# Optimization experiments

Measured on AMD Instinct MI355X. Metric: run time of the kernel, lower is better.

The kernel has to match this reference:

```python
import jax, jax.numpy as jnp
import numpy as np

N_NODES = 100000
N_EDGES = 500000
D = 128          # node / edge latent size
HIDDEN = 128     # MLP hidden width


def setup_inputs() -> dict:
    key = jax.random.key(0)
    k = jax.random.split(key, 10)
    node_attr = jax.random.normal(k[0], (N_NODES, D), dtype=jnp.float32)
    edge_attr = jax.random.normal(k[1], (N_EDGES, D), dtype=jnp.float32)
    senders_idx = jax.random.randint(k[2], (N_EDGES,), 0, N_NODES, dtype=jnp.int64 if jax.config.jax_enable_x64 else jnp.int32).astype(jnp.int32)
    receivers_idx = jax.random.randint(k[3], (N_EDGES,), 0, N_NODES).astype(jnp.int32)
    in_dim = 3 * D  # sender + receiver + edge feats
    s1 = 1.0 / np.sqrt(in_dim)
    s2 = 1.0 / np.sqrt(HIDDEN)
    W1 = jax.random.uniform(k[4], (in_dim, HIDDEN), minval=-s1, maxval=s1, dtype=jnp.float32)
    b1 = jnp.zeros((HIDDEN,), jnp.float32)
    W2 = jax.random.uniform(k[5], (HIDDEN, D), minval=-s2, maxval=s2, dtype=jnp.float32)
    b2 = jnp.zeros((D,), jnp.float32)
    ln_gamma = jnp.ones((D,), jnp.float32)
    ln_beta = jnp.zeros((D,), jnp.float32)
    return {
        "node_attr": node_attr, "edge_attr": edge_attr,
        "senders_idx": senders_idx, "receivers_idx": receivers_idx,
        "W1": W1, "b1": b1, "W2": W2, "b2": b2,
        "ln_gamma": ln_gamma, "ln_beta": ln_beta,
    }


def _layer_norm(x, gamma, beta, eps=1e-5):
    mu = jnp.mean(x, axis=-1, keepdims=True)
    var = jnp.var(x, axis=-1, keepdims=True)
    return (x - mu) * jax.lax.rsqrt(var + eps) * gamma + beta


def reference(node_attr, edge_attr, senders_idx, receivers_idx,
              W1, b1, W2, b2, ln_gamma, ln_beta):
    # Gather sender/receiver node features  [E, D] each
    senders_attr = node_attr[senders_idx]
    receivers_attr = node_attr[receivers_idx]
    # Concat -> [E, 3D]
    collected = jnp.concatenate([senders_attr, receivers_attr, edge_attr], axis=1)
    # MLP with ReLU + output LayerNorm (MeshGraphNets custom_func)
    h = jax.nn.relu(collected @ W1 + b1)
    out = h @ W2 + b2
    new_edge_attr = _layer_norm(out, ln_gamma, ln_beta)
    return new_edge_attr
```

## Files before the change

kernel.cpp:

```cpp
#include <hip/hip_runtime.h>

#define D 128
#define NEDGES 500000
#define NNODES 100000

typedef short short8 __attribute__((ext_vector_type(8)));
typedef float f32x4 __attribute__((ext_vector_type(4)));
typedef unsigned short us4 __attribute__((ext_vector_type(4)));
typedef unsigned short us8 __attribute__((ext_vector_type(8)));

static __device__ __forceinline__ unsigned short f2bf(float f) {
  unsigned u = __builtin_bit_cast(unsigned, f);
  u += 0x7fff + ((u >> 16) & 1);
  return (unsigned short)(u >> 16);
}

static __device__ __forceinline__ unsigned short f2h(float f) {
  return __builtin_bit_cast(unsigned short, (_Float16)f);
}

static __device__ __forceinline__ float h2f(unsigned short u) {
  return (float)__builtin_bit_cast(_Float16, u);
}

static __device__ __forceinline__ short8 cvt8v(f32x4 a, f32x4 b) {
  short8 r;
  r[0] = (short)f2bf(a[0]); r[1] = (short)f2bf(a[1]);
  r[2] = (short)f2bf(a[2]); r[3] = (short)f2bf(a[3]);
  r[4] = (short)f2bf(b[0]); r[5] = (short)f2bf(b[1]);
  r[6] = (short)f2bf(b[2]); r[7] = (short)f2bf(b[3]);
  return r;
}

__global__ void prep_weights2(const float* __restrict__ W1,
                              const float* __restrict__ W2,
                              unsigned short* __restrict__ WnS,
                              unsigned short* __restrict__ WnR,
                              unsigned short* __restrict__ WnE,
                              unsigned short* __restrict__ Wt2) {
  int tid = blockIdx.x * 256 + threadIdx.x;
  int seg = tid >> 14;
  int t = tid & 16383;
  int unit = t >> 7;
  int k = t & 127;
  if (seg == 0)      WnS[t] = f2bf(W1[k * 128 + unit]);
  else if (seg == 1) WnR[t] = f2bf(W1[(128 + k) * 128 + unit]);
  else if (seg == 2) WnE[t] = f2bf(W1[(256 + k) * 128 + unit]);
  else {
    int kk = k >> 5, rem = k & 31, q = rem >> 3, s = rem & 7;
    int keff = ((s < 4) ? (2 * kk) : (2 * kk + 1)) * 16 + q * 4 + (s & 3);
    Wt2[t] = f2bf(W2[keff * 128 + unit]);
  }
}

__global__ __launch_bounds__(512) void node_proj(
    const float* __restrict__ node,
    const unsigned short* __restrict__ WnS,
    const unsigned short* __restrict__ WnR,
    unsigned short* __restrict__ Ps,
    unsigned short* __restrict__ Pr) {
  __shared__ __align__(16) unsigned short wlds[2][16384];
  {
    const us8* s0 = (const us8*)WnS;
    const us8* s1 = (const us8*)WnR;
#pragma unroll
    for (int c = 0; c < 4; ++c) {
      int g = threadIdx.x + c * 512;
      int row = g >> 4, slot = g & 15;
      int dst = row * 128 + ((slot ^ (row & 7)) << 3);
      *(us8*)&wlds[0][dst] = s0[g];
      *(us8*)&wlds[1][dst] = s1[g];
    }
  }
  __syncthreads();

  const int lane = threadIdx.x & 63;
  const int wave = threadIdx.x >> 6;
  const int col = lane & 15;
  const int quad = lane >> 4;
  const int c7 = col & 7;
  const int nBase = blockIdx.x * 128 + wave * 16;
  if (nBase >= NNODES) return;

  const float* src = node + (size_t)(nBase + col) * D + quad * 8;
  f32x4 c[4][2];
#pragma unroll
  for (int kk = 0; kk < 4; ++kk) {
    c[kk][0] = __builtin_nontemporal_load((const f32x4*)(src + kk * 32));
    c[kk][1] = __builtin_nontemporal_load((const f32x4*)(src + kk * 32 + 4));
  }
  f32x4 accS[8], accR[8];
  const f32x4 zero = {0.f, 0.f, 0.f, 0.f};
#pragma unroll
  for (int m = 0; m < 8; ++m) { accS[m] = zero; accR[m] = zero; }

#pragma unroll
  for (int kk = 0; kk < 4; ++kk) {
    short8 bf = cvt8v(c[kk][0], c[kk][1]);
#pragma unroll
    for (int m = 0; m < 8; ++m) {
      const int off = (m * 16 + col) * 128 + (((kk * 4 + quad) ^ c7) << 3);
      short8 as = *(const short8*)&wlds[0][off];
      accS[m] = __builtin_amdgcn_mfma_f32_16x16x32_bf16(as, bf, accS[m], 0, 0, 0);
      short8 ar = *(const short8*)&wlds[1][off];
      accR[m] = __builtin_amdgcn_mfma_f32_16x16x32_bf16(ar, bf, accR[m], 0, 0, 0);
    }
  }

  unsigned short* ps = Ps + (size_t)(nBase + col) * D + quad * 32;
  unsigned short* pr = Pr + (size_t)(nBase + col) * D + quad * 32;
#pragma unroll
  for (int m = 0; m < 8; m += 2) {
    us8 w1v, w2v;
#pragma unroll
    for (int r = 0; r < 4; ++r) {
      w1v[r] = f2h(accS[m][r]);     w1v[4 + r] = f2h(accS[m + 1][r]);
      w2v[r] = f2h(accR[m][r]);     w2v[4 + r] = f2h(accR[m + 1][r]);
    }
    *(us8*)(ps + m * 4) = w1v;
    *(us8*)(pr + m * 4) = w2v;
  }
}

__global__ __launch_bounds__(512) void edge_mlp(
    const float* __restrict__ edge,
    const int* __restrict__ send, const int* __restrict__ recv,
    const unsigned short* __restrict__ WnE,
    const unsigned short* __restrict__ Wt2,
    const unsigned short* __restrict__ Ps,
    const unsigned short* __restrict__ Pr,
    const float* __restrict__ b1, const float* __restrict__ b2,
    const float* __restrict__ gamma, const float* __restrict__ beta,
    float* __restrict__ out) {
  __shared__ __align__(16) unsigned short wlds[2][16384];
  {
    const us8* s0 = (const us8*)WnE;
    const us8* s1 = (const us8*)Wt2;
#pragma unroll
    for (int c = 0; c < 4; ++c) {
      int g = threadIdx.x + c * 512;
      int row = g >> 4, slot = g & 15;
      int dst = row * 128 + ((slot ^ (row & 7)) << 3);
      *(us8*)&wlds[0][dst] = s0[g];
      *(us8*)&wlds[1][dst] = s1[g];
    }
  }
  __syncthreads();

  const int lane = threadIdx.x & 63;
  const int wave = threadIdx.x >> 6;
  const int col = lane & 15;
  const int quad = lane >> 4;
  const int q4 = quad * 4;
  const int c7 = col & 7;
  const int eBase = blockIdx.x * 128 + wave * 16;
  if (eBase >= NEDGES) return;

  const int e = eBase + col;
  const int si = send[e];
  const int ri = recv[e];

  const float* ge = edge + (size_t)e * D + quad * 8;
  f32x4 c[4][2];
#pragma unroll
  for (int kk = 0; kk < 4; ++kk) {
    c[kk][0] = __builtin_nontemporal_load((const f32x4*)(ge + kk * 32));
    c[kk][1] = __builtin_nontemporal_load((const f32x4*)(ge + kk * 32 + 4));
  }

  const us8* ps = (const us8*)(Ps + (size_t)si * D + quad * 32);
  const us8* pr = (const us8*)(Pr + (size_t)ri * D + quad * 32);
  us8 gs[4], gr[4];
#pragma unroll
  for (int i = 0; i < 4; ++i) { gs[i] = ps[i]; gr[i] = pr[i]; }

  f32x4 acc[8];
#pragma unroll
  for (int m = 0; m < 8; ++m)
    acc[m] = *(const f32x4*)(b1 + m * 16 + q4);

#pragma unroll
  for (int kk = 0; kk < 4; ++kk) {
    short8 bf = cvt8v(c[kk][0], c[kk][1]);
#pragma unroll
    for (int m = 0; m < 8; ++m) {
      const int off = (m * 16 + col) * 128 + (((kk * 4 + quad) ^ c7) << 3);
      short8 af = *(const short8*)&wlds[0][off];
      acc[m] = __builtin_amdgcn_mfma_f32_16x16x32_bf16(af, bf, acc[m], 0, 0, 0);
    }
  }

  short8 hb[4];
#pragma unroll
  for (int m = 0; m < 8; ++m) {
    const int i = m >> 1, b = (m & 1) * 4;
    f32x4 v = acc[m];
#pragma unroll
    for (int r = 0; r < 4; ++r)
      v[r] += h2f(gs[i][b + r]) + h2f(gr[i][b + r]);
#pragma unroll
    for (int r = 0; r < 4; ++r)
      hb[i][b + r] = (short)f2bf(fmaxf(v[r], 0.f));
  }

  f32x4 acc2[8];
#pragma unroll
  for (int m = 0; m < 8; ++m)
    acc2[m] = *(const f32x4*)(b2 + m * 16 + q4);
#pragma unroll
  for (int kk = 0; kk < 4; ++kk) {
#pragma unroll
    for (int m = 0; m < 8; ++m) {
      const int off = (m * 16 + col) * 128 + (((kk * 4 + quad) ^ c7) << 3);
      short8 af = *(const short8*)&wlds[1][off];
      acc2[m] = __builtin_amdgcn_mfma_f32_16x16x32_bf16(af, hb[kk], acc2[m], 0, 0, 0);
    }
  }

  float s = 0.f, ss = 0.f;
#pragma unroll
  for (int m = 0; m < 8; ++m)
#pragma unroll
    for (int r = 0; r < 4; ++r) {
      float v = acc2[m][r];
      s += v; ss += v * v;
    }
  s += __shfl_xor(s, 16);  s += __shfl_xor(s, 32);
  ss += __shfl_xor(ss, 16); ss += __shfl_xor(ss, 32);
  const float mean = s * (1.f / 128.f);
  const float var = ss * (1.f / 128.f) - mean * mean;
  const float rstd = rsqrtf(var + 1e-5f);
  float* op = out + (size_t)e * D;
#pragma unroll
  for (int m = 0; m < 8; ++m) {
    f32x4 gv = *(const f32x4*)(gamma + m * 16 + q4);
    f32x4 bv = *(const f32x4*)(beta + m * 16 + q4);
    f32x4 o;
#pragma unroll
    for (int r = 0; r < 4; ++r)
      o[r] = (acc2[m][r] - mean) * rstd * gv[r] + bv[r];
    __builtin_nontemporal_store(o, (f32x4*)(op + m * 16 + q4));
  }
}


__global__ void prep_weights(const float* __restrict__ W1,
                             const float* __restrict__ W2,
                             unsigned short* __restrict__ Wt1,
                             unsigned short* __restrict__ Wt2) {
  int tid = blockIdx.x * 256 + threadIdx.x;
  if (tid < 128 * 384) {
    int h = tid / 384, k = tid % 384;
    Wt1[tid] = f2bf(W1[k * 128 + h]);
  } else {
    int t2 = tid - 128 * 384;
    if (t2 < 128 * 128) {
      int o = t2 / 128, h = t2 % 128;
      Wt2[t2] = f2bf(W2[h * 128 + o]);
    }
  }
}

__global__ __launch_bounds__(256, 4) void edge_kernel(
    const float* __restrict__ node, const float* __restrict__ edge,
    const int* __restrict__ send, const int* __restrict__ recv,
    const unsigned short* __restrict__ Wt1,
    const unsigned short* __restrict__ Wt2,
    const float* __restrict__ b1, const float* __restrict__ b2,
    const float* __restrict__ gamma, const float* __restrict__ beta,
    float* __restrict__ out) {
  __shared__ unsigned short hbuf[4][32][136];

  const int lane = threadIdx.x & 63;
  const int wave = threadIdx.x >> 6;
  const int col = lane & 15;
  const int quad = lane >> 4;
  const int q4 = quad * 4;
  const int eBase = blockIdx.x * 128 + wave * 32;
  const bool active = eBase < NEDGES;

  if (active) {
    const int e0 = eBase + col;
    const int e1 = eBase + 16 + col;
    const float* g0s = node + (size_t)send[e0] * D;
    const float* g0r = node + (size_t)recv[e0] * D;
    const float* g0e = edge + (size_t)e0 * D;
    const float* g1s = node + (size_t)send[e1] * D;
    const float* g1r = node + (size_t)recv[e1] * D;
    const float* g1e = edge + (size_t)e1 * D;

    f32x4 acc[2][8];
#pragma unroll
    for (int m = 0; m < 8; ++m) {
      f32x4 bv = *(const f32x4*)(b1 + m * 16 + q4);
      acc[0][m] = bv; acc[1][m] = bv;
    }

    f32x4 pl[2][2][2];
#define SRC0(seg) ((seg) == 0 ? g0s : (seg) == 1 ? g0r : g0e)
#define SRC1(seg) ((seg) == 0 ? g1s : (seg) == 1 ? g1r : g1e)
#define ISSUE(kk, slot)                                         \
    {                                                           \
      const int seg_ = (kk) >> 2;                               \
      const int ks_ = ((kk) & 3) * 32 + quad * 8;               \
      pl[slot][0][0] = *(const f32x4*)(SRC0(seg_) + ks_);       \
      pl[slot][0][1] = *(const f32x4*)(SRC0(seg_) + ks_ + 4);   \
      pl[slot][1][0] = *(const f32x4*)(SRC1(seg_) + ks_);       \
      pl[slot][1][1] = *(const f32x4*)(SRC1(seg_) + ks_ + 4);   \
    }

    ISSUE(0, 0)
    ISSUE(1, 1)
#pragma unroll
    for (int kk = 0; kk < 12; ++kk) {
      const int slot = kk & 1;
      short8 bf0 = cvt8v(pl[slot][0][0], pl[slot][0][1]);
      short8 bf1 = cvt8v(pl[slot][1][0], pl[slot][1][1]);
      if (kk + 2 < 12) ISSUE(kk + 2, slot)
      const int kfull = kk * 32 + quad * 8;
#pragma unroll
      for (int m = 0; m < 8; ++m) {
        short8 af = *(const short8*)(Wt1 + (size_t)(m * 16 + col) * 384 + kfull);
        acc[0][m] = __builtin_amdgcn_mfma_f32_16x16x32_bf16(af, bf0, acc[0][m], 0, 0, 0);
        acc[1][m] = __builtin_amdgcn_mfma_f32_16x16x32_bf16(af, bf1, acc[1][m], 0, 0, 0);
      }
    }
#undef ISSUE
#undef SRC0
#undef SRC1

#pragma unroll
    for (int g = 0; g < 2; ++g) {
#pragma unroll
      for (int m = 0; m < 8; ++m) {
        f32x4 v = acc[g][m];
        us4 w;
        w.x = f2bf(v[0] > 0.f ? v[0] : 0.f);
        w.y = f2bf(v[1] > 0.f ? v[1] : 0.f);
        w.z = f2bf(v[2] > 0.f ? v[2] : 0.f);
        w.w = f2bf(v[3] > 0.f ? v[3] : 0.f);
        *(us4*)&hbuf[wave][g * 16 + col][m * 16 + q4] = w;
      }
    }
  }

  __syncthreads();

  if (active) {
    f32x4 acc2[2][8];
#pragma unroll
    for (int m = 0; m < 8; ++m) {
      f32x4 bv = *(const f32x4*)(b2 + m * 16 + q4);
      acc2[0][m] = bv; acc2[1][m] = bv;
    }
#pragma unroll
    for (int kk = 0; kk < 4; ++kk) {
      const int kb = kk * 32 + quad * 8;
      short8 bf0 = *(const short8*)&hbuf[wave][col][kb];
      short8 bf1 = *(const short8*)&hbuf[wave][16 + col][kb];
#pragma unroll
      for (int m = 0; m < 8; ++m) {
        short8 af = *(const short8*)(Wt2 + (size_t)(m * 16 + col) * 128 + kb);
        acc2[0][m] = __builtin_amdgcn_mfma_f32_16x16x32_bf16(af, bf0, acc2[0][m], 0, 0, 0);
        acc2[1][m] = __builtin_amdgcn_mfma_f32_16x16x32_bf16(af, bf1, acc2[1][m], 0, 0, 0);
      }
    }
#pragma unroll
    for (int g = 0; g < 2; ++g) {
      float s = 0.f, ss = 0.f;
#pragma unroll
      for (int m = 0; m < 8; ++m) {
#pragma unroll
        for (int r = 0; r < 4; ++r) {
          float v = acc2[g][m][r];
          s += v; ss += v * v;
        }
      }
      s += __shfl_xor(s, 16);  s += __shfl_xor(s, 32);
      ss += __shfl_xor(ss, 16); ss += __shfl_xor(ss, 32);
      const float mean = s * (1.f / 128.f);
      const float var = ss * (1.f / 128.f) - mean * mean;
      const float rstd = rsqrtf(var + 1e-5f);
      const int e = eBase + g * 16 + col;
      float* op = out + (size_t)e * D;
#pragma unroll
      for (int m = 0; m < 8; ++m) {
        f32x4 gv = *(const f32x4*)(gamma + m * 16 + q4);
        f32x4 bv = *(const f32x4*)(beta + m * 16 + q4);
        f32x4 o;
#pragma unroll
        for (int r = 0; r < 4; ++r)
          o[r] = (acc2[g][m][r] - mean) * rstd * gv[r] + bv[r];
        *(f32x4*)(op + m * 16 + q4) = o;
      }
    }
  }
}

extern "C" void kernel_launch(void* const* d_in, const int* in_sizes, int n_in,
                              void* d_out, int out_size, void* d_ws, size_t ws_size,
                              hipStream_t stream) {
  const float* node  = (const float*)d_in[0];
  const float* edge  = (const float*)d_in[1];
  const int*   send  = (const int*)d_in[2];
  const int*   recv  = (const int*)d_in[3];
  const float* W1    = (const float*)d_in[4];
  const float* b1    = (const float*)d_in[5];
  const float* W2    = (const float*)d_in[6];
  const float* b2    = (const float*)d_in[7];
  const float* gam   = (const float*)d_in[8];
  const float* bet   = (const float*)d_in[9];
  float* out = (float*)d_out;

  const size_t wbytes = (size_t)4 * 128 * 128 * sizeof(unsigned short);
  const size_t pbytes = (size_t)2 * NNODES * D * sizeof(unsigned short);

  if (ws_size >= wbytes + pbytes) {
    unsigned short* WnS = (unsigned short*)d_ws;
    unsigned short* WnR = WnS + 128 * 128;
    unsigned short* WnE = WnR + 128 * 128;
    unsigned short* Wt2 = WnE + 128 * 128;
    unsigned short* Ps  = Wt2 + 128 * 128;
    unsigned short* Pr  = Ps + (size_t)NNODES * D;

    prep_weights2<<<256, 256, 0, stream>>>(W1, W2, WnS, WnR, WnE, Wt2);
    node_proj<<<(NNODES + 127) / 128, 512, 0, stream>>>(node, WnS, WnR, Ps, Pr);
    edge_mlp<<<(NEDGES + 127) / 128, 512, 0, stream>>>(edge, send, recv, WnE, Wt2,
                                                       Ps, Pr, b1, b2, gam, bet, out);
  } else {
    unsigned short* Wt1 = (unsigned short*)d_ws;
    unsigned short* Wt2 = Wt1 + 128 * 384;
    prep_weights<<<256, 256, 0, stream>>>(W1, W2, Wt1, Wt2);
    const int nblocks = (NEDGES + 127) / 128;
    edge_kernel<<<nblocks, 256, 0, stream>>>(node, edge, send, recv, Wt1, Wt2,
                                             b1, b2, gam, bet, out);
  }
}
```

Measured before the change: 538.5 us.

## Make edge_mlp persistent with software-pipelined prefetch of next tile's inputs

Turns edge_mlp into a persistent kernel: a fixed grid of 512 blocks where each wave loops over 16-edge tiles with a grid stride. While the current tile is computed, it prefetches the next tile's edge features, the gathered node projections and the indices two tiles ahead. Biases and LayerNorm parameters move into shared memory so they are loaded once per block, and the launch bounds ask for 4 blocks per CU. This amortises the per-block weight staging into LDS and hides gather latency, at the cost of more register pressure from the double-buffered loads.

After: 1.277 ms. 2.37x slower.

```diff
diff --git a/kernel.cpp b/kernel.cpp
--- a/kernel.cpp
+++ b/kernel.cpp
@@ -122,7 +122,7 @@
   }
 }
 
-__global__ __launch_bounds__(512) void edge_mlp(
+__global__ __launch_bounds__(512, 4) void edge_mlp(
     const float* __restrict__ edge,
     const int* __restrict__ send, const int* __restrict__ recv,
     const unsigned short* __restrict__ WnE,
@@ -133,6 +133,7 @@
     const float* __restrict__ gamma, const float* __restrict__ beta,
     float* __restrict__ out) {
   __shared__ __align__(16) unsigned short wlds[2][16384];
+  __shared__ __align__(16) float cbias[4][128];
   {
     const us8* s0 = (const us8*)WnE;
     const us8* s1 = (const us8*)Wt2;
@@ -144,6 +145,11 @@
       *(us8*)&wlds[0][dst] = s0[g];
       *(us8*)&wlds[1][dst] = s1[g];
     }
+    int which = threadIdx.x >> 7, j = threadIdx.x & 127;
+    if (which == 0)      cbias[0][j] = b1[j];
+    else if (which == 1) cbias[1][j] = b2[j];
+    else if (which == 2) cbias[2][j] = gamma[j];
+    else                 cbias[3][j] = beta[j];
   }
   __syncthreads();
 
@@ -153,93 +159,135 @@
   const int quad = lane >> 4;
   const int q4 = quad * 4;
   const int c7 = col & 7;
-  const int eBase = blockIdx.x * 128 + wave * 16;
-  if (eBase >= NEDGES) return;
-
-  const int e = eBase + col;
-  const int si = send[e];
-  const int ri = recv[e];
-
-  const float* ge = edge + (size_t)e * D + quad * 8;
+
+  const int NW = gridDim.x * 8;
+  const int NT = NEDGES / 16;
+  const int gw = blockIdx.x * 8 + wave;
+  if (gw >= NT) return;
+  const int last = gw + ((NT - 1 - gw) / NW) * NW;
+
+  int t = gw;
+  int e = t * 16 + col;
+  int si = send[e];
+  int ri = recv[e];
+
   f32x4 c[4][2];
-#pragma unroll
-  for (int kk = 0; kk < 4; ++kk) {
-    c[kk][0] = __builtin_nontemporal_load((const f32x4*)(ge + kk * 32));
-    c[kk][1] = __builtin_nontemporal_load((const f32x4*)(ge + kk * 32 + 4));
-  }
-
-  const us8* ps = (const us8*)(Ps + (size_t)si * D + quad * 32);
-  const us8* pr = (const us8*)(Pr + (size_t)ri * D + quad * 32);
+  {
+    const float* ge = edge + (size_t)e * D + quad * 8;
+#pragma unroll
+    for (int kk = 0; kk < 4; ++kk) {
+      c[kk][0] = __builtin_nontemporal_load((const f32x4*)(ge + kk * 32));
+      c[kk][1] = __builtin_nontemporal_load((const f32x4*)(ge + kk * 32 + 4));
+    }
+  }
   us8 gs[4], gr[4];
-#pragma unroll
-  for (int i = 0; i < 4; ++i) { gs[i] = ps[i]; gr[i] = pr[i]; }
-
-  f32x4 acc[8];
-#pragma unroll
-  for (int m = 0; m < 8; ++m)
-    acc[m] = *(const f32x4*)(b1 + m * 16 + q4);
-
-#pragma unroll
-  for (int kk = 0; kk < 4; ++kk) {
-    short8 bf = cvt8v(c[kk][0], c[kk][1]);
+  {
+    const us8* ps = (const us8*)(Ps + (size_t)si * D + quad * 32);
+    const us8* pr = (const us8*)(Pr + (size_t)ri * D + quad * 32);
+#pragma unroll
+    for (int i = 0; i < 4; ++i) { gs[i] = ps[i]; gr[i] = pr[i]; }
+  }
+  int tn = (t < last) ? t + NW : last;
+  int en = tn * 16 + col;
+  int sin = send[en];
+  int rin = recv[en];
+
+  for (;;) {
+    short8 bf[4];
+#pragma unroll
+    for (int kk = 0; kk < 4; ++kk) bf[kk] = cvt8v(c[kk][0], c[kk][1]);
+
+    {
+      const float* gen = edge + (size_t)en * D + quad * 8;
+#pragma unroll
+      for (int kk = 0; kk < 4; ++kk) {
+        c[kk][0] = __builtin_nontemporal_load((const f32x4*)(gen + kk * 32));
+        c[kk][1] = __builtin_nontemporal_load((const f32x4*)(gen + kk * 32 + 4));
+      }
+    }
+
+    f32x4 acc[8];
+#pragma unroll
+    for (int m = 0; m < 8; ++m)
+      acc[m] = *(const f32x4*)&cbias[0][m * 16 + q4];
+#pragma unroll
+    for (int kk = 0; kk < 4; ++kk) {
+#pragma unroll
+      for (int m = 0; m < 8; ++m) {
+        const int off = (m * 16 + col) * 128 + (((kk * 4 + quad) ^ c7) << 3);
+        short8 af = *(const short8*)&wlds[0][off];
+        acc[m] = __builtin_amdgcn_mfma_f32_16x16x32_bf16(af, bf[kk], acc[m], 0, 0, 0);
+      }
+    }
+
+    short8 hb[4];
 #pragma unroll
     for (int m = 0; m < 8; ++m) {
-      const int off = (m * 16 + col) * 128 + (((kk * 4 + quad) ^ c7) << 3);
-      short8 af = *(const short8*)&wlds[0][off];
-      acc[m] = __builtin_amdgcn_mfma_f32_16x16x32_bf16(af, bf, acc[m], 0, 0, 0);
-    }
-  }
-
-  short8 hb[4];
-#pragma unroll
-  for (int m = 0; m < 8; ++m) {
-    const int i = m >> 1, b = (m & 1) * 4;
-    f32x4 v = acc[m];
-#pragma unroll
-    for (int r = 0; r < 4; ++r)
-      v[r] += h2f(gs[i][b + r]) + h2f(gr[i][b + r]);
-#pragma unroll
-    for (int r = 0; r < 4; ++r)
-      hb[i][b + r] = (short)f2bf(fmaxf(v[r], 0.f));
-  }
-
-  f32x4 acc2[8];
-#pragma unroll
-  for (int m = 0; m < 8; ++m)
-    acc2[m] = *(const f32x4*)(b2 + m * 16 + q4);
-#pragma unroll
-  for (int kk = 0; kk < 4; ++kk) {
+      const int i = m >> 1, b = (m & 1) * 4;
+      f32x4 v = acc[m];
+#pragma unroll
+      for (int r = 0; r < 4; ++r)
+        v[r] += h2f(gs[i][b + r]) + h2f(gr[i][b + r]);
+#pragma unroll
+      for (int r = 0; r < 4; ++r)
+        hb[i][b + r] = (short)f2bf(fmaxf(v[r], 0.f));
+    }
+
+    {
+      const us8* psn = (const us8*)(Ps + (size_t)sin * D + quad * 32);
+      const us8* prn = (const us8*)(Pr + (size_t)rin * D + quad * 32);
+#pragma unroll
+      for (int i = 0; i < 4; ++i) { gs[i] = psn[i]; gr[i] = prn[i]; }
+    }
+
+    const int tnn = (tn < last) ? tn + NW : last;
+    const int enn = tnn * 16 + col;
+    const int sin2 = send[enn];
+    const int rin2 = recv[enn];
+
+    f32x4 acc2[8];
+#pragma unroll
+    for (int m = 0; m < 8; ++m)
+      acc2[m] = *(const f32x4*)&cbias[1][m * 16 + q4];
+#pragma unroll
+    for (int kk = 0; kk < 4; ++kk) {
+#pragma unroll
+      for (int m = 0; m < 8; ++m) {
+        const int off = (m * 16 + col) * 128 + (((kk * 4 + quad) ^ c7) << 3);
+        short8 af = *(const short8*)&wlds[1][off];
+        acc2[m] = __builtin_amdgcn_mfma_f32_16x16x32_bf16(af, hb[kk], acc2[m], 0, 0, 0);
+      }
+    }
+
+    float s = 0.f, ss = 0.f;
+#pragma unroll
+    for (int m = 0; m < 8; ++m)
+#pragma unroll
+      for (int r = 0; r < 4; ++r) {
+        float v = acc2[m][r];
+        s += v; ss += v * v;
+      }
+    s += __shfl_xor(s, 16);  s += __shfl_xor(s, 32);
+    ss += __shfl_xor(ss, 16); ss += __shfl_xor(ss, 32);
+    const float mean = s * (1.f / 128.f);
+    const float var = ss * (1.f / 128.f) - mean * mean;
+    const float rstd = rsqrtf(var + 1e-5f);
+    float* op = out + (size_t)e * D;
 #pragma unroll
     for (int m = 0; m < 8; ++m) {
-      const int off = (m * 16 + col) * 128 + (((kk * 4 + quad) ^ c7) << 3);
-      short8 af = *(const short8*)&wlds[1][off];
-      acc2[m] = __builtin_amdgcn_mfma_f32_16x16x32_bf16(af, hb[kk], acc2[m], 0, 0, 0);
-    }
-  }
-
-  float s = 0.f, ss = 0.f;
-#pragma unroll
-  for (int m = 0; m < 8; ++m)
-#pragma unroll
-    for (int r = 0; r < 4; ++r) {
-      float v = acc2[m][r];
-      s += v; ss += v * v;
-    }
-  s += __shfl_xor(s, 16);  s += __shfl_xor(s, 32);
-  ss += __shfl_xor(ss, 16); ss += __shfl_xor(ss, 32);
-  const float mean = s * (1.f / 128.f);
-  const float var = ss * (1.f / 128.f) - mean * mean;
-  const float rstd = rsqrtf(var + 1e-5f);
-  float* op = out + (size_t)e * D;
-#pragma unroll
-  for (int m = 0; m < 8; ++m) {
-    f32x4 gv = *(const f32x4*)(gamma + m * 16 + q4);
-    f32x4 bv = *(const f32x4*)(beta + m * 16 + q4);
-    f32x4 o;
-#pragma unroll
-    for (int r = 0; r < 4; ++r)
-      o[r] = (acc2[m][r] - mean) * rstd * gv[r] + bv[r];
-    __builtin_nontemporal_store(o, (f32x4*)(op + m * 16 + q4));
+      f32x4 gv = *(const f32x4*)&cbias[2][m * 16 + q4];
+      f32x4 bv = *(const f32x4*)&cbias[3][m * 16 + q4];
+      f32x4 o;
+#pragma unroll
+      for (int r = 0; r < 4; ++r)
+        o[r] = (acc2[m][r] - mean) * rstd * gv[r] + bv[r];
+      __builtin_nontemporal_store(o, (f32x4*)(op + m * 16 + q4));
+    }
+
+    if (t == last) break;
+    t = tn; e = en;
+    tn = tnn; en = enn;
+    sin = sin2; rin = rin2;
   }
 }
 
@@ -425,8 +473,8 @@
 
     prep_weights2<<<256, 256, 0, stream>>>(W1, W2, WnS, WnR, WnE, Wt2);
     node_proj<<<(NNODES + 127) / 128, 512, 0, stream>>>(node, WnS, WnR, Ps, Pr);
-    edge_mlp<<<(NEDGES + 127) / 128, 512, 0, stream>>>(edge, send, recv, WnE, Wt2,
-                                                       Ps, Pr, b1, b2, gam, bet, out);
+    edge_mlp<<<512, 512, 0, stream>>>(edge, send, recv, WnE, Wt2,
+                                      Ps, Pr, b1, b2, gam, bet, out);
   } else {
     unsigned short* Wt1 = (unsigned short*)d_ws;
     unsigned short* Wt2 = Wt1 + 128 * 384;
```
